# Kernel tuning notes

Measured on AMD Instinct MI355X. Metric: run time of the kernel, lower is better.

The kernel has to match this reference:

```python
import jax, jax.numpy as jnp
import numpy as np

B, S, H, A = 2, 1024, 512, 128


def setup_inputs() -> dict:
    key = jax.random.key(0)
    k1, k2, k3, k4 = jax.random.split(key, 4)
    lstm_output = jax.random.normal(k1, (B, S, H), dtype=jnp.float32)
    w = jax.random.normal(k2, (H, A), dtype=jnp.float32) / np.sqrt(H)
    u = jax.random.normal(k3, (H, A), dtype=jnp.float32) / np.sqrt(H)
    v = jax.random.normal(k4, (A,), dtype=jnp.float32) / np.sqrt(A)
    return {"lstm_output": lstm_output, "w": w, "u": u, "v": v}


def reference(lstm_output, w, u, v):
    # lstm_output: (B,S,H); w,u: (H,A); v: (A,)
    wx = jnp.einsum('bsh,ha->bsa', lstm_output, w)   # (B,S,A)
    ux = jnp.einsum('bsh,ha->bsa', lstm_output, u)   # (B,S,A)
    # e[b,i,j] = tanh(wx[b,i] + ux[b,j]) . v  -> (B,S,S), via (B,S,S,A) intermediate
    e = jnp.einsum('bija,a->bij', jnp.tanh(wx[:, :, None, :] + ux[:, None, :, :]), v)
    attention_weights = jax.nn.softmax(e, axis=-1)   # (B,S,S)
    # bmm(attn, lstm_output) -> (B,S,H), then sum over dim 1 -> (B,H)
    context_vector = jnp.einsum('bij,bjh->bh', attention_weights, lstm_output)
    return context_vector, attention_weights
```

## Files before the change

kernel.cpp:

```cpp
#include <hip/hip_runtime.h>

#define HH   512
#define AA   128
#define SB   1024
#define BATCH 2

__device__ __forceinline__ float fast_rcp(float x) { return __builtin_amdgcn_rcpf(x); }
__device__ __forceinline__ float fast_ex2(float x) { return __builtin_amdgcn_exp2f(x); }

__global__ __launch_bounds__(256) void k1_gemm(const float* __restrict__ lstm,
                                               const float* __restrict__ w,
                                               const float* __restrict__ u,
                                               float* __restrict__ part0,
                                               float* __restrict__ part1,
                                               float* __restrict__ colw)
{
    __shared__ float As[32][68];
    __shared__ float Bs[32][36];
    const int t  = threadIdx.x;
    const int bx = blockIdx.x, by = blockIdx.y, bz = blockIdx.z;
    const int m0 = bx * 64;
    const int n0 = by * 32;
    const float* __restrict__ Bsrc = (n0 < AA) ? w : u;
    const int ncol = n0 & (AA - 1);

    if (bx == 0 && by == 0) {
        float4 z4; z4.x = z4.y = z4.z = z4.w = 0.f;
        ((float4*)colw)[bz * 256 + t] = z4;
    }

    const int r  = t & 63;
    const int kq = (t >> 6) * 8;
    const int kk = t >> 3;
    const int nq = (t & 7) * 4;
    const int tm = t >> 4;
    const int tn = t & 15;

    float acc[4][2];
    #pragma unroll
    for (int i = 0; i < 4; ++i) { acc[i][0] = 0.f; acc[i][1] = 0.f; }

    for (int kc = 0; kc < 8; ++kc) {
        const int k0 = bz * 256 + kc * 32;
        const float* ap = &lstm[(size_t)(m0 + r) * HH + k0 + kq];
        const float4 a0 = *(const float4*)&ap[0];
        const float4 a1 = *(const float4*)&ap[4];
        As[kq + 0][r] = a0.x; As[kq + 1][r] = a0.y;
        As[kq + 2][r] = a0.z; As[kq + 3][r] = a0.w;
        As[kq + 4][r] = a1.x; As[kq + 5][r] = a1.y;
        As[kq + 6][r] = a1.z; As[kq + 7][r] = a1.w;
        const float4 bv = *(const float4*)&Bsrc[(size_t)(k0 + kk) * AA + ncol + nq];
        *(float4*)&Bs[kk][nq] = bv;
        __syncthreads();
        #pragma unroll
        for (int k = 0; k < 32; ++k) {
            const float4 av = *(const float4*)&As[k][4 * tm];
            const float2 bb = *(const float2*)&Bs[k][2 * tn];
            acc[0][0] = fmaf(av.x, bb.x, acc[0][0]);
            acc[0][1] = fmaf(av.x, bb.y, acc[0][1]);
            acc[1][0] = fmaf(av.y, bb.x, acc[1][0]);
            acc[1][1] = fmaf(av.y, bb.y, acc[1][1]);
            acc[2][0] = fmaf(av.z, bb.x, acc[2][0]);
            acc[2][1] = fmaf(av.z, bb.y, acc[2][1]);
            acc[3][0] = fmaf(av.w, bb.x, acc[3][0]);
            acc[3][1] = fmaf(av.w, bb.y, acc[3][1]);
        }
        __syncthreads();
    }

    float* __restrict__ part = bz ? part1 : part0;
    #pragma unroll
    for (int mi = 0; mi < 4; ++mi) {
        float2 st; st.x = acc[mi][0]; st.y = acc[mi][1];
        *(float2*)&part[(size_t)(m0 + 4 * tm + mi) * 256 + n0 + 2 * tn] = st;
    }
}

__global__ __launch_bounds__(256) void k1b_combine_exp(const float* __restrict__ part0,
                                                       const float* __restrict__ part1,
                                                       float* __restrict__ P,
                                                       float* __restrict__ Q)
{
    const float KK = 2.8853900817779268f;
    const int idx = blockIdx.x * 256 + threadIdx.x;
    const float4 c0 = ((const float4*)part0)[idx];
    const float4 c1 = ((const float4*)part1)[idx];
    float4 o;
    o.x = fast_ex2(KK * (c0.x + c1.x));
    o.y = fast_ex2(KK * (c0.y + c1.y));
    o.z = fast_ex2(KK * (c0.z + c1.z));
    o.w = fast_ex2(KK * (c0.w + c1.w));
    const int m  = idx >> 6;
    const int qd = idx & 63;
    float* dst = (qd < 32) ? &P[(size_t)m * AA + qd * 4]
                           : &Q[(size_t)m * AA + (qd - 32) * 4];
    *(float4*)dst = o;
}

__global__ __launch_bounds__(1024) void k2_fused(const float* __restrict__ P,
                                                 const float* __restrict__ Q,
                                                 const float* __restrict__ v,
                                                 float* __restrict__ attn,
                                                 float* __restrict__ colw,
                                                 float* __restrict__ ctx)
{
    const int b  = blockIdx.y;
    const int i0 = blockIdx.x * 8;
    const int j  = threadIdx.x;

    if (blockIdx.x == 0 && j < HH) ctx[b * HH + j] = 0.f;

    const float* __restrict__ Qrow = &Q[((size_t)b * SB + j) * AA];
    const float* __restrict__ Pb   = &P[((size_t)b * SB + i0) * AA];

    float acc[8];
    #pragma unroll
    for (int i = 0; i < 8; ++i) acc[i] = 0.f;
    float Vacc = 0.f;

    #pragma unroll 2
    for (int x = 0; x < 32; ++x) {
        const float4 q4 = *(const float4*)&Qrow[x * 4];
        const float4 vv = *(const float4*)&v[x * 4];
        Vacc += (vv.x + vv.y) + (vv.z + vv.w);
        #pragma unroll
        for (int i = 0; i < 8; ++i) {
            const float4 p = *(const float4*)&Pb[i * AA + x * 4];
            const float d0 = fmaf(p.x, q4.x, 1.0f);
            const float d1 = fmaf(p.y, q4.y, 1.0f);
            const float d2 = fmaf(p.z, q4.z, 1.0f);
            const float d3 = fmaf(p.w, q4.w, 1.0f);
            const float na = fmaf(vv.y, d0, vv.x * d1);
            const float nb = fmaf(vv.w, d2, vv.z * d3);
            const float ra = fast_rcp(d0 * d1);
            const float rb = fast_rcp(d2 * d3);
            acc[i] = fmaf(na, ra, acc[i]);
            acc[i] = fmaf(nb, rb, acc[i]);
        }
    }

    const float L2E  = 1.4426950408889634f;
    const float base = Vacc * L2E;
    float E[8];
    #pragma unroll
    for (int i = 0; i < 8; ++i)
        E[i] = fast_ex2(fmaf(acc[i], -2.0f * L2E, base));

    __shared__ float red[8][16];
    const int lane = j & 63, wv = j >> 6;
    #pragma unroll
    for (int i = 0; i < 8; ++i) {
        float s = E[i];
        #pragma unroll
        for (int off = 32; off > 0; off >>= 1) s += __shfl_xor(s, off);
        if (lane == 0) red[i][wv] = s;
    }
    __syncthreads();

    float csum = 0.f;
    float* __restrict__ arow = &attn[((size_t)b * SB + i0) * SB + j];
    #pragma unroll
    for (int i = 0; i < 8; ++i) {
        const float4* rr = (const float4*)red[i];
        const float4 r0 = rr[0], r1 = rr[1], r2 = rr[2], r3 = rr[3];
        const float rs = ((r0.x + r0.y) + (r0.z + r0.w)) + ((r1.x + r1.y) + (r1.z + r1.w))
                       + ((r2.x + r2.y) + (r2.z + r2.w)) + ((r3.x + r3.y) + (r3.z + r3.w));
        const float a = E[i] * fast_rcp(rs);
        arow[(size_t)i * SB] = a;
        csum += a;
    }
    atomicAdd(&colw[b * SB + j], csum);
}

__global__ __launch_bounds__(256) void k4_context(const float* __restrict__ lstm,
                                                  const float* __restrict__ colw,
                                                  float* __restrict__ ctx)
{
    const int b  = blockIdx.z;
    const int h  = blockIdx.x * 256 + threadIdx.x;
    const int j0 = blockIdx.y * 128;
    __shared__ float cw[128];
    if (threadIdx.x < 128) cw[threadIdx.x] = colw[b * SB + j0 + threadIdx.x];
    __syncthreads();
    float acc = 0.f;
    #pragma unroll 8
    for (int jj = 0; jj < 128; ++jj)
        acc = fmaf(cw[jj], lstm[(size_t)(b * SB + j0 + jj) * HH + h], acc);
    atomicAdd(&ctx[b * HH + h], acc);
}

extern "C" void kernel_launch(void* const* d_in, const int* in_sizes, int n_in,
                              void* d_out, int out_size, void* d_ws, size_t ws_size,
                              hipStream_t stream)
{
    const float* lstm = (const float*)d_in[0];
    const float* w    = (const float*)d_in[1];
    const float* u    = (const float*)d_in[2];
    const float* v    = (const float*)d_in[3];

    float* out  = (float*)d_out;
    float* ctx  = out;
    float* attn = out + BATCH * HH;

    float* part0 = (float*)d_ws;
    float* part1 = part0 + (size_t)2048 * 256;
    float* P     = part1 + (size_t)2048 * 256;
    float* Qb    = P     + (size_t)BATCH * SB * AA;
    float* colw  = Qb    + (size_t)BATCH * SB * AA;

    k1_gemm<<<dim3(32, 8, 2), 256, 0, stream>>>(lstm, w, u, part0, part1, colw);
    k1b_combine_exp<<<dim3(512), 256, 0, stream>>>(part0, part1, P, Qb);
    k2_fused<<<dim3(128, BATCH), 1024, 0, stream>>>(P, Qb, v, attn, colw, ctx);
    k4_context<<<dim3(2, 8, BATCH), 256, 0, stream>>>(lstm, colw, ctx);
}
```

Measured before the change: 62.95 us.

## Merge reciprocals in attention score loop, retile k2 and register-only GEMM

In the fused score kernel, the two reciprocals per four-element group are merged into one by cross-multiplying the numerators, so each group needs a single fast_rcp. The kernel is retiled to 512-thread blocks that each handle 4 query rows and two key columns per thread, which halves the P reads per key. The first GEMM drops LDS staging: each wave reads A rows straight into registers and broadcasts B loads from global memory. Products of four denominators could overflow for large inputs, and the GEMM now leans on cache for B reuse instead of shared memory.

```diff
diff --git a/kernel.cpp b/kernel.cpp
--- a/kernel.cpp
+++ b/kernel.cpp
@@ -15,65 +15,57 @@
                                                float* __restrict__ part1,
                                                float* __restrict__ colw)
 {
-    __shared__ float As[32][68];
-    __shared__ float Bs[32][36];
-    const int t  = threadIdx.x;
+    const int t    = threadIdx.x;
+    const int lane = t & 63;
+    const int wv   = __builtin_amdgcn_readfirstlane(t >> 6);
     const int bx = blockIdx.x, by = blockIdx.y, bz = blockIdx.z;
-    const int m0 = bx * 64;
-    const int n0 = by * 32;
+    const int m0 = bx * 128;
+    const int n0 = by * 16 + wv * 4;
     const float* __restrict__ Bsrc = (n0 < AA) ? w : u;
-    const int ncol = n0 & (AA - 1);
+    const int nc = n0 & (AA - 1);
 
     if (bx == 0 && by == 0) {
         float4 z4; z4.x = z4.y = z4.z = z4.w = 0.f;
         ((float4*)colw)[bz * 256 + t] = z4;
     }
 
-    const int r  = t & 63;
-    const int kq = (t >> 6) * 8;
-    const int kk = t >> 3;
-    const int nq = (t & 7) * 4;
-    const int tm = t >> 4;
-    const int tn = t & 15;
-
-    float acc[4][2];
-    #pragma unroll
-    for (int i = 0; i < 4; ++i) { acc[i][0] = 0.f; acc[i][1] = 0.f; }
-
-    for (int kc = 0; kc < 8; ++kc) {
-        const int k0 = bz * 256 + kc * 32;
-        const float* ap = &lstm[(size_t)(m0 + r) * HH + k0 + kq];
-        const float4 a0 = *(const float4*)&ap[0];
-        const float4 a1 = *(const float4*)&ap[4];
-        As[kq + 0][r] = a0.x; As[kq + 1][r] = a0.y;
-        As[kq + 2][r] = a0.z; As[kq + 3][r] = a0.w;
-        As[kq + 4][r] = a1.x; As[kq + 5][r] = a1.y;
-        As[kq + 6][r] = a1.z; As[kq + 7][r] = a1.w;
-        const float4 bv = *(const float4*)&Bsrc[(size_t)(k0 + kk) * AA + ncol + nq];
-        *(float4*)&Bs[kk][nq] = bv;
-        __syncthreads();
-        #pragma unroll
-        for (int k = 0; k < 32; ++k) {
-            const float4 av = *(const float4*)&As[k][4 * tm];
-            const float2 bb = *(const float2*)&Bs[k][2 * tn];
-            acc[0][0] = fmaf(av.x, bb.x, acc[0][0]);
-            acc[0][1] = fmaf(av.x, bb.y, acc[0][1]);
-            acc[1][0] = fmaf(av.y, bb.x, acc[1][0]);
-            acc[1][1] = fmaf(av.y, bb.y, acc[1][1]);
-            acc[2][0] = fmaf(av.z, bb.x, acc[2][0]);
-            acc[2][1] = fmaf(av.z, bb.y, acc[2][1]);
-            acc[3][0] = fmaf(av.w, bb.x, acc[3][0]);
-            acc[3][1] = fmaf(av.w, bb.y, acc[3][1]);
+    const int kz0 = bz * 256;
+    const float* __restrict__ Arow0 = &lstm[(size_t)(m0 + lane) * HH + kz0];
+    const float* __restrict__ Arow1 = Arow0 + (size_t)64 * HH;
+
+    float acc0[4], acc1[4];
+    #pragma unroll
+    for (int c = 0; c < 4; ++c) { acc0[c] = 0.f; acc1[c] = 0.f; }
+
+    for (int c = 0; c < 16; ++c) {
+        const int kb = c * 16;
+        float a0r[16], a1r[16];
+        #pragma unroll
+        for (int q = 0; q < 4; ++q) {
+            *(float4*)&a0r[q * 4] = *(const float4*)&Arow0[kb + q * 4];
+            *(float4*)&a1r[q * 4] = *(const float4*)&Arow1[kb + q * 4];
         }
-        __syncthreads();
+        #pragma unroll
+        for (int k = 0; k < 16; ++k) {
+            const float4 bq = *(const float4*)&Bsrc[(size_t)(kz0 + kb + k) * AA + nc];
+            const float a0 = a0r[k];
+            const float a1 = a1r[k];
+            acc0[0] = fmaf(a0, bq.x, acc0[0]);
+            acc0[1] = fmaf(a0, bq.y, acc0[1]);
+            acc0[2] = fmaf(a0, bq.z, acc0[2]);
+            acc0[3] = fmaf(a0, bq.w, acc0[3]);
+            acc1[0] = fmaf(a1, bq.x, acc1[0]);
+            acc1[1] = fmaf(a1, bq.y, acc1[1]);
+            acc1[2] = fmaf(a1, bq.z, acc1[2]);
+            acc1[3] = fmaf(a1, bq.w, acc1[3]);
+        }
     }
 
     float* __restrict__ part = bz ? part1 : part0;
-    #pragma unroll
-    for (int mi = 0; mi < 4; ++mi) {
-        float2 st; st.x = acc[mi][0]; st.y = acc[mi][1];
-        *(float2*)&part[(size_t)(m0 + 4 * tm + mi) * 256 + n0 + 2 * tn] = st;
-    }
+    float4 s0; s0.x = acc0[0]; s0.y = acc0[1]; s0.z = acc0[2]; s0.w = acc0[3];
+    float4 s1; s1.x = acc1[0]; s1.y = acc1[1]; s1.z = acc1[2]; s1.w = acc1[3];
+    *(float4*)&part[(size_t)(m0 + lane)      * 256 + n0] = s0;
+    *(float4*)&part[(size_t)(m0 + lane + 64) * 256 + n0] = s1;
 }
 
 __global__ __launch_bounds__(256) void k1b_combine_exp(const float* __restrict__ part0,
@@ -97,79 +89,101 @@
     *(float4*)dst = o;
 }
 
-__global__ __launch_bounds__(1024) void k2_fused(const float* __restrict__ P,
-                                                 const float* __restrict__ Q,
-                                                 const float* __restrict__ v,
-                                                 float* __restrict__ attn,
-                                                 float* __restrict__ colw,
-                                                 float* __restrict__ ctx)
+__global__ __launch_bounds__(512) void k2_fused(const float* __restrict__ P,
+                                                const float* __restrict__ Q,
+                                                const float* __restrict__ v,
+                                                float* __restrict__ attn,
+                                                float* __restrict__ colw,
+                                                float* __restrict__ ctx)
 {
     const int b  = blockIdx.y;
-    const int i0 = blockIdx.x * 8;
-    const int j  = threadIdx.x;
-
-    if (blockIdx.x == 0 && j < HH) ctx[b * HH + j] = 0.f;
-
-    const float* __restrict__ Qrow = &Q[((size_t)b * SB + j) * AA];
-    const float* __restrict__ Pb   = &P[((size_t)b * SB + i0) * AA];
-
-    float acc[8];
-    #pragma unroll
-    for (int i = 0; i < 8; ++i) acc[i] = 0.f;
+    const int i0 = blockIdx.x * 4;
+    const int t  = threadIdx.x;
+
+    if (blockIdx.x == 0) ctx[b * HH + t] = 0.f;
+
+    const float* __restrict__ Qr0 = &Q[((size_t)b * SB + t)       * AA];
+    const float* __restrict__ Qr1 = &Q[((size_t)b * SB + t + 512) * AA];
+    const float* __restrict__ Pb  = &P[((size_t)b * SB + i0)      * AA];
+
+    float acc[4][2];
+    #pragma unroll
+    for (int i = 0; i < 4; ++i) { acc[i][0] = 0.f; acc[i][1] = 0.f; }
     float Vacc = 0.f;
 
     #pragma unroll 2
     for (int x = 0; x < 32; ++x) {
-        const float4 q4 = *(const float4*)&Qrow[x * 4];
+        const float4 q0 = *(const float4*)&Qr0[x * 4];
+        const float4 q1 = *(const float4*)&Qr1[x * 4];
         const float4 vv = *(const float4*)&v[x * 4];
         Vacc += (vv.x + vv.y) + (vv.z + vv.w);
         #pragma unroll
-        for (int i = 0; i < 8; ++i) {
+        for (int i = 0; i < 4; ++i) {
             const float4 p = *(const float4*)&Pb[i * AA + x * 4];
-            const float d0 = fmaf(p.x, q4.x, 1.0f);
-            const float d1 = fmaf(p.y, q4.y, 1.0f);
-            const float d2 = fmaf(p.z, q4.z, 1.0f);
-            const float d3 = fmaf(p.w, q4.w, 1.0f);
-            const float na = fmaf(vv.y, d0, vv.x * d1);
-            const float nb = fmaf(vv.w, d2, vv.z * d3);
-            const float ra = fast_rcp(d0 * d1);
-            const float rb = fast_rcp(d2 * d3);
-            acc[i] = fmaf(na, ra, acc[i]);
-            acc[i] = fmaf(nb, rb, acc[i]);
+            {
+                const float d0 = fmaf(p.x, q0.x, 1.0f);
+                const float d1 = fmaf(p.y, q0.y, 1.0f);
+                const float d2 = fmaf(p.z, q0.z, 1.0f);
+                const float d3 = fmaf(p.w, q0.w, 1.0f);
+                const float p01 = d0 * d1, p23 = d2 * d3;
+                const float na = fmaf(vv.x, d1, vv.y * d0);
+                const float nb = fmaf(vv.z, d3, vv.w * d2);
+                const float N  = fmaf(nb, p01, na * p23);
+                const float r  = fast_rcp(p01 * p23);
+                acc[i][0] = fmaf(N, r, acc[i][0]);
+            }
+            {
+                const float d0 = fmaf(p.x, q1.x, 1.0f);
+                const float d1 = fmaf(p.y, q1.y, 1.0f);
+                const float d2 = fmaf(p.z, q1.z, 1.0f);
+                const float d3 = fmaf(p.w, q1.w, 1.0f);
+                const float p01 = d0 * d1, p23 = d2 * d3;
+                const float na = fmaf(vv.x, d1, vv.y * d0);
+                const float nb = fmaf(vv.z, d3, vv.w * d2);
+                const float N  = fmaf(nb, p01, na * p23);
+                const float r  = fast_rcp(p01 * p23);
+                acc[i][1] = fmaf(N, r, acc[i][1]);
+            }
         }
     }
 
     const float L2E  = 1.4426950408889634f;
     const float base = Vacc * L2E;
-    float E[8];
-    #pragma unroll
-    for (int i = 0; i < 8; ++i)
-        E[i] = fast_ex2(fmaf(acc[i], -2.0f * L2E, base));
-
-    __shared__ float red[8][16];
-    const int lane = j & 63, wv = j >> 6;
-    #pragma unroll
-    for (int i = 0; i < 8; ++i) {
-        float s = E[i];
+    float E[4][2];
+    #pragma unroll
+    for (int i = 0; i < 4; ++i) {
+        E[i][0] = fast_ex2(fmaf(acc[i][0], -2.0f * L2E, base));
+        E[i][1] = fast_ex2(fmaf(acc[i][1], -2.0f * L2E, base));
+    }
+
+    __shared__ float red[4][8];
+    const int lane = t & 63, wvi = t >> 6;
+    #pragma unroll
+    for (int i = 0; i < 4; ++i) {
+        float s = E[i][0] + E[i][1];
         #pragma unroll
         for (int off = 32; off > 0; off >>= 1) s += __shfl_xor(s, off);
-        if (lane == 0) red[i][wv] = s;
+        if (lane == 0) red[i][wvi] = s;
     }
     __syncthreads();
 
-    float csum = 0.f;
-    float* __restrict__ arow = &attn[((size_t)b * SB + i0) * SB + j];
-    #pragma unroll
-    for (int i = 0; i < 8; ++i) {
+    float csum0 = 0.f, csum1 = 0.f;
+    float* __restrict__ arow = &attn[((size_t)b * SB + i0) * SB];
+    #pragma unroll
+    for (int i = 0; i < 4; ++i) {
         const float4* rr = (const float4*)red[i];
-        const float4 r0 = rr[0], r1 = rr[1], r2 = rr[2], r3 = rr[3];
-        const float rs = ((r0.x + r0.y) + (r0.z + r0.w)) + ((r1.x + r1.y) + (r1.z + r1.w))
-                       + ((r2.x + r2.y) + (r2.z + r2.w)) + ((r3.x + r3.y) + (r3.z + r3.w));
-        const float a = E[i] * fast_rcp(rs);
-        arow[(size_t)i * SB] = a;
-        csum += a;
-    }
-    atomicAdd(&colw[b * SB + j], csum);
+        const float4 r0 = rr[0], r1 = rr[1];
+        const float rs = ((r0.x + r0.y) + (r0.z + r0.w)) + ((r1.x + r1.y) + (r1.z + r1.w));
+        const float inv = fast_rcp(rs);
+        const float a0 = E[i][0] * inv;
+        const float a1 = E[i][1] * inv;
+        arow[(size_t)i * SB + t]       = a0;
+        arow[(size_t)i * SB + t + 512] = a1;
+        csum0 += a0;
+        csum1 += a1;
+    }
+    atomicAdd(&colw[b * SB + t],       csum0);
+    atomicAdd(&colw[b * SB + t + 512], csum1);
 }
 
 __global__ __launch_bounds__(256) void k4_context(const float* __restrict__ lstm,
@@ -208,8 +222,8 @@
     float* Qb    = P     + (size_t)BATCH * SB * AA;
     float* colw  = Qb    + (size_t)BATCH * SB * AA;
 
-    k1_gemm<<<dim3(32, 8, 2), 256, 0, stream>>>(lstm, w, u, part0, part1, colw);
+    k1_gemm<<<dim3(16, 16, 2), 256, 0, stream>>>(lstm, w, u, part0, part1, colw);
     k1b_combine_exp<<<dim3(512), 256, 0, stream>>>(part0, part1, P, Qb);
-    k2_fused<<<dim3(128, BATCH), 1024, 0, stream>>>(P, Qb, v, attn, colw, ctx);
+    k2_fused<<<dim3(256, BATCH), 512, 0, stream>>>(P, Qb, v, attn, colw, ctx);
     k4_context<<<dim3(2, 8, BATCH), 256, 0, stream>>>(lstm, colw, ctx);
 }
```

Result: slower. 92.07 us (+46.3%).

## Split score kernel into exp-score and scale passes with single reciprocal per quad

Applied to the files above, without the earlier changes.

Replaces the fused 1024-thread score/softmax kernel with two kernels. The first writes unnormalized exponentials to the attention output and accumulates row sums atomically. The second rescales each row and accumulates column sums. The new score kernel keeps P and v in shared memory, computes two j-columns per thread, and merges four tanh terms under one reciprocal instead of two, cutting rcp work. In exchange it adds an extra read-modify-write pass over the 8 MB attention matrix, plus atomics and an additional launch.

```diff
diff --git a/kernel.cpp b/kernel.cpp
--- a/kernel.cpp
+++ b/kernel.cpp
@@ -8,12 +8,30 @@
 __device__ __forceinline__ float fast_rcp(float x) { return __builtin_amdgcn_rcpf(x); }
 __device__ __forceinline__ float fast_ex2(float x) { return __builtin_amdgcn_exp2f(x); }
 
+__device__ __forceinline__ void quad_acc(const float4 p, const float4 q4,
+                                         const float4 vv, float& acc)
+{
+    const float d0 = fmaf(p.x, q4.x, 1.0f);
+    const float d1 = fmaf(p.y, q4.y, 1.0f);
+    const float d2 = fmaf(p.z, q4.z, 1.0f);
+    const float d3 = fmaf(p.w, q4.w, 1.0f);
+    const float p01 = d0 * d1, p23 = d2 * d3;
+    const float na = fmaf(vv.x, d1, vv.y * d0);
+    const float nb = fmaf(vv.z, d3, vv.w * d2);
+    const float N  = fmaf(na, p23, nb * p01);
+    acc = fmaf(N, fast_rcp(p01 * p23), acc);
+}
+
 __global__ __launch_bounds__(256) void k1_gemm(const float* __restrict__ lstm,
                                                const float* __restrict__ w,
                                                const float* __restrict__ u,
+                                               const float* __restrict__ v,
                                                float* __restrict__ part0,
                                                float* __restrict__ part1,
-                                               float* __restrict__ colw)
+                                               float* __restrict__ rsum,
+                                               float* __restrict__ colw,
+                                               float* __restrict__ ctx,
+                                               float* __restrict__ vsum)
 {
     __shared__ float As[32][68];
     __shared__ float Bs[32][36];
@@ -25,8 +43,19 @@
     const int ncol = n0 & (AA - 1);
 
     if (bx == 0 && by == 0) {
-        float4 z4; z4.x = z4.y = z4.z = z4.w = 0.f;
-        ((float4*)colw)[bz * 256 + t] = z4;
+        #pragma unroll
+        for (int r = 0; r < 4; ++r) {
+            rsum[bz * 1024 + r * 256 + t] = 0.f;
+            colw[bz * 1024 + r * 256 + t] = 0.f;
+        }
+        ctx[bz * 512 + t]       = 0.f;
+        ctx[bz * 512 + 256 + t] = 0.f;
+        if (bz == 0 && t < 64) {
+            float s = v[t] + v[t + 64];
+            #pragma unroll
+            for (int off = 32; off > 0; off >>= 1) s += __shfl_xor(s, off);
+            if (t == 0) vsum[0] = s;
+        }
     }
 
     const int r  = t & 63;
@@ -97,76 +126,86 @@
     *(float4*)dst = o;
 }
 
-__global__ __launch_bounds__(1024) void k2_fused(const float* __restrict__ P,
-                                                 const float* __restrict__ Q,
-                                                 const float* __restrict__ v,
-                                                 float* __restrict__ attn,
-                                                 float* __restrict__ colw,
-                                                 float* __restrict__ ctx)
-{
-    const int b  = blockIdx.y;
-    const int i0 = blockIdx.x * 8;
-    const int j  = threadIdx.x;
-
-    if (blockIdx.x == 0 && j < HH) ctx[b * HH + j] = 0.f;
-
-    const float* __restrict__ Qrow = &Q[((size_t)b * SB + j) * AA];
-    const float* __restrict__ Pb   = &P[((size_t)b * SB + i0) * AA];
-
-    float acc[8];
-    #pragma unroll
-    for (int i = 0; i < 8; ++i) acc[i] = 0.f;
-    float Vacc = 0.f;
-
-    #pragma unroll 2
-    for (int x = 0; x < 32; ++x) {
-        const float4 q4 = *(const float4*)&Qrow[x * 4];
-        const float4 vv = *(const float4*)&v[x * 4];
-        Vacc += (vv.x + vv.y) + (vv.z + vv.w);
-        #pragma unroll
-        for (int i = 0; i < 8; ++i) {
-            const float4 p = *(const float4*)&Pb[i * AA + x * 4];
-            const float d0 = fmaf(p.x, q4.x, 1.0f);
-            const float d1 = fmaf(p.y, q4.y, 1.0f);
-            const float d2 = fmaf(p.z, q4.z, 1.0f);
-            const float d3 = fmaf(p.w, q4.w, 1.0f);
-            const float na = fmaf(vv.y, d0, vv.x * d1);
-            const float nb = fmaf(vv.w, d2, vv.z * d3);
-            const float ra = fast_rcp(d0 * d1);
-            const float rb = fast_rcp(d2 * d3);
-            acc[i] = fmaf(na, ra, acc[i]);
-            acc[i] = fmaf(nb, rb, acc[i]);
+__global__ __launch_bounds__(256) void k2a_escore(const float* __restrict__ P,
+                                                  const float* __restrict__ Q,
+                                                  const float* __restrict__ v,
+                                                  const float* __restrict__ vsum,
+                                                  float* __restrict__ E,
+                                                  float* __restrict__ rsum)
+{
+    __shared__ float Pl[4 * AA];
+    __shared__ float vl[AA];
+    const int b  = blockIdx.z;
+    const int i0 = blockIdx.y * 4;
+    const int jb = blockIdx.x * 512;
+    const int t  = threadIdx.x;
+
+    if (t < 128)      ((float4*)Pl)[t] = ((const float4*)&P[((size_t)b * SB + i0) * AA])[t];
+    else if (t < 160) ((float4*)vl)[t - 128] = ((const float4*)v)[t - 128];
+    __syncthreads();
+
+    const int j0 = jb + t;
+    const float4* __restrict__ Qr0 = (const float4*)&Q[((size_t)b * SB + j0) * AA];
+    const float4* __restrict__ Qr1 = (const float4*)&Q[((size_t)b * SB + j0 + 256) * AA];
+
+    float acc[4][2];
+    #pragma unroll
+    for (int i = 0; i < 4; ++i) { acc[i][0] = 0.f; acc[i][1] = 0.f; }
+
+    #pragma unroll 1
+    for (int xc = 0; xc < 8; ++xc) {
+        float4 qa0 = Qr0[xc * 4 + 0], qa1 = Qr0[xc * 4 + 1];
+        float4 qa2 = Qr0[xc * 4 + 2], qa3 = Qr0[xc * 4 + 3];
+        float4 qb0 = Qr1[xc * 4 + 0], qb1 = Qr1[xc * 4 + 1];
+        float4 qb2 = Qr1[xc * 4 + 2], qb3 = Qr1[xc * 4 + 3];
+        #pragma unroll
+        for (int x2 = 0; x2 < 4; ++x2) {
+            const float4 qa = (x2 == 0) ? qa0 : (x2 == 1) ? qa1 : (x2 == 2) ? qa2 : qa3;
+            const float4 qb = (x2 == 0) ? qb0 : (x2 == 1) ? qb1 : (x2 == 2) ? qb2 : qb3;
+            const int off = (xc * 4 + x2) * 4;
+            const float4 vv = *(const float4*)&vl[off];
+            #pragma unroll
+            for (int i = 0; i < 4; ++i) {
+                const float4 p = *(const float4*)&Pl[i * AA + off];
+                quad_acc(p, qa, vv, acc[i][0]);
+                quad_acc(p, qb, vv, acc[i][1]);
+            }
         }
     }
 
     const float L2E  = 1.4426950408889634f;
-    const float base = Vacc * L2E;
-    float E[8];
-    #pragma unroll
-    for (int i = 0; i < 8; ++i)
-        E[i] = fast_ex2(fmaf(acc[i], -2.0f * L2E, base));
-
-    __shared__ float red[8][16];
-    const int lane = j & 63, wv = j >> 6;
+    const float base = vsum[0] * L2E;
+    float* __restrict__ Eout = &E[((size_t)(b * SB + i0)) * SB + j0];
+    const int lane = t & 63;
+    #pragma unroll
+    for (int i = 0; i < 4; ++i) {
+        const float e0 = fast_ex2(fmaf(acc[i][0], -2.0f * L2E, base));
+        const float e1 = fast_ex2(fmaf(acc[i][1], -2.0f * L2E, base));
+        Eout[(size_t)i * SB]       = e0;
+        Eout[(size_t)i * SB + 256] = e1;
+        float s = e0 + e1;
+        #pragma unroll
+        for (int off = 32; off > 0; off >>= 1) s += __shfl_xor(s, off);
+        if (lane == 0) atomicAdd(&rsum[b * SB + i0 + i], s);
+    }
+}
+
+__global__ __launch_bounds__(256) void k2b_scale_colsum(float* __restrict__ attn,
+                                                        const float* __restrict__ rsum,
+                                                        float* __restrict__ colw)
+{
+    const int b  = blockIdx.z;
+    const int i0 = blockIdx.y * 8;
+    const int j  = blockIdx.x * 256 + threadIdx.x;
+
+    float csum = 0.f;
     #pragma unroll
     for (int i = 0; i < 8; ++i) {
-        float s = E[i];
-        #pragma unroll
-        for (int off = 32; off > 0; off >>= 1) s += __shfl_xor(s, off);
-        if (lane == 0) red[i][wv] = s;
-    }
-    __syncthreads();
-
-    float csum = 0.f;
-    float* __restrict__ arow = &attn[((size_t)b * SB + i0) * SB + j];
-    #pragma unroll
-    for (int i = 0; i < 8; ++i) {
-        const float4* rr = (const float4*)red[i];
-        const float4 r0 = rr[0], r1 = rr[1], r2 = rr[2], r3 = rr[3];
-        const float rs = ((r0.x + r0.y) + (r0.z + r0.w)) + ((r1.x + r1.y) + (r1.z + r1.w))
-                       + ((r2.x + r2.y) + (r2.z + r2.w)) + ((r3.x + r3.y) + (r3.z + r3.w));
-        const float a = E[i] * fast_rcp(rs);
-        arow[(size_t)i * SB] = a;
+        const int row = b * SB + i0 + i;
+        const float inv = fast_rcp(rsum[row]);
+        float* __restrict__ ap = &attn[(size_t)row * SB + j];
+        const float a = (*ap) * inv;
+        *ap = a;
         csum += a;
     }
     atomicAdd(&colw[b * SB + j], csum);
@@ -206,10 +245,14 @@
     float* part1 = part0 + (size_t)2048 * 256;
     float* P     = part1 + (size_t)2048 * 256;
     float* Qb    = P     + (size_t)BATCH * SB * AA;
-    float* colw  = Qb    + (size_t)BATCH * SB * AA;
-
-    k1_gemm<<<dim3(32, 8, 2), 256, 0, stream>>>(lstm, w, u, part0, part1, colw);
+    float* rsum  = Qb    + (size_t)BATCH * SB * AA;
+    float* colw  = rsum  + (size_t)BATCH * SB;
+    float* vsum  = colw  + (size_t)BATCH * SB;
+
+    k1_gemm<<<dim3(32, 8, 2), 256, 0, stream>>>(lstm, w, u, v, part0, part1,
+                                                rsum, colw, ctx, vsum);
     k1b_combine_exp<<<dim3(512), 256, 0, stream>>>(part0, part1, P, Qb);
-    k2_fused<<<dim3(128, BATCH), 1024, 0, stream>>>(P, Qb, v, attn, colw, ctx);
+    k2a_escore<<<dim3(2, 256, BATCH), 256, 0, stream>>>(P, Qb, v, vsum, attn, rsum);
+    k2b_scale_colsum<<<dim3(4, 128, BATCH), 256, 0, stream>>>(attn, rsum, colw);
     k4_context<<<dim3(2, 8, BATCH), 256, 0, stream>>>(lstm, colw, ctx);
 }
```

Result: slower. 80.27 us (+27.5%).
